# Kernel tuning notes

Measured on AMD Instinct MI355X. Metric: run time of the kernel, lower is better.

## Reference

```python
import jax, jax.numpy as jnp
import numpy as np
from math import sqrt

DIM, RANK = 1024, 32
B, S = 4, 4096

def setup_inputs() -> dict:
    key = jax.random.key(0)
    kx, kq, kk, kv = jax.random.split(key, 4)
    # xavier_uniform bounds
    bq = sqrt(6.0 / (RANK + DIM))
    bv = sqrt(6.0 / (DIM + DIM))
    return {
        "x": jax.random.normal(kx, (B, S, DIM), dtype=jnp.float32),
        "Q": jax.random.uniform(kq, (RANK, DIM), jnp.float32, -bq, bq),
        "K": jax.random.uniform(kk, (RANK, DIM), jnp.float32, -bq, bq),
        "VO": jax.random.uniform(kv, (DIM, DIM), jnp.float32, -bv, bv),
    }

def reference(x, Q, K, VO):
    d = x.shape[-1]
    # low-rank projections: [b,t,r] each (avoid materializing QK^T [d,d] or 4-way einsum blowup)
    xq = jnp.einsum('btd,rd->btr', x, Q)
    xk = jnp.einsum('bud,rd->bur', x, K)
    scores = jnp.einsum('btr,bur->btu', xq, xk) / sqrt(d)
    attn = jax.nn.softmax(scores, axis=2)
    # value aggregation then output projection
    ctx = jnp.einsum('btu,bud->btd', attn, x)
    return jnp.einsum('btd,de->bte', ctx, VO)
```

## Files before the change

### kernel.cpp

```cpp
#include <hip/hip_runtime.h>
#include <hip/hip_bf16.h>

#define DIM  1024
#define RANK 32
#define BATCH 4
#define SEQ  4096
#define MTOT (BATCH * SEQ)

typedef short bf16x8 __attribute__((ext_vector_type(8)));
typedef float f32x4 __attribute__((ext_vector_type(4)));
typedef float f32x16 __attribute__((ext_vector_type(16)));
typedef unsigned short ushort8v __attribute__((ext_vector_type(8)));
typedef unsigned int uint2v __attribute__((ext_vector_type(2)));

__device__ inline unsigned short f2bf(float f) {
    union { float f; unsigned int u; } v; v.f = f;
    return (unsigned short)((v.u + 0x7FFFu + ((v.u >> 16) & 1u)) >> 16);
}

__device__ inline unsigned int pk_bf16(float a, float b) {
    __hip_bfloat162 h = __float22bfloat162_rn(make_float2(a, b));
    unsigned int u; __builtin_memcpy(&u, &h, 4);
    return u;
}

__device__ inline void gl_lds16(const unsigned short* g, unsigned short* l) {
    __builtin_amdgcn_global_load_lds(
        (const __attribute__((address_space(1))) unsigned int*)g,
        (__attribute__((address_space(3))) unsigned int*)l, 16, 0, 0);
}

__global__ __launch_bounds__(256) void k_cvt_qk(const float* __restrict__ Q,
                                                const float* __restrict__ K,
                                                unsigned short* __restrict__ wqk) {
    int i = blockIdx.x * 256 + threadIdx.x;
    int row = i >> 10, col = i & 1023;
    const float SC = 0.045084220027779984f;
    float v = (row < RANK) ? Q[row * DIM + col] * SC : K[(row - RANK) * DIM + col];
    wqk[i] = f2bf(v);
}

__global__ __launch_bounds__(256) void k_transpose_cvt(const float* __restrict__ in,
                                                       unsigned short* __restrict__ out,
                                                       int R, int C) {
    __shared__ float tile[64][65];
    const int tid = threadIdx.x;
    const int c0 = blockIdx.x * 64, r0 = blockIdx.y * 64;
    {
        int c = (tid & 15) * 4;
#pragma unroll
        for (int i = 0; i < 4; ++i) {
            int r = (tid >> 4) + i * 16;
            f32x4 v = *(const f32x4*)(in + (size_t)(r0 + r) * C + c0 + c);
            tile[r][c + 0] = v[0]; tile[r][c + 1] = v[1];
            tile[r][c + 2] = v[2]; tile[r][c + 3] = v[3];
        }
    }
    __syncthreads();
    {
        int r = (tid & 15) * 4;
#pragma unroll
        for (int i = 0; i < 4; ++i) {
            int c = (tid >> 4) + i * 16;
            unsigned short o0 = f2bf(tile[r + 0][c]), o1 = f2bf(tile[r + 1][c]);
            unsigned short o2 = f2bf(tile[r + 2][c]), o3 = f2bf(tile[r + 3][c]);
            unsigned short* p = out + (size_t)(c0 + c) * R + r0 + r;
            p[0] = o0; p[1] = o1; p[2] = o2; p[3] = o3;
        }
    }
}

__global__ __launch_bounds__(256) void k_xbf(const float* __restrict__ x,
                                             unsigned short* __restrict__ xbf) {
    size_t i = ((size_t)blockIdx.x * 256 + threadIdx.x) * 8;
    f32x4 v0 = *(const f32x4*)(x + i);
    f32x4 v1 = *(const f32x4*)(x + i + 4);
    ushort8v o;
    o[0] = f2bf(v0[0]); o[1] = f2bf(v0[1]); o[2] = f2bf(v0[2]); o[3] = f2bf(v0[3]);
    o[4] = f2bf(v1[0]); o[5] = f2bf(v1[1]); o[6] = f2bf(v1[2]); o[7] = f2bf(v1[3]);
    *(ushort8v*)(xbf + i) = o;
}

__global__ __launch_bounds__(256) void k_proj(const unsigned short* __restrict__ xbf,
                                              const unsigned short* __restrict__ wqk,
                                              unsigned short* __restrict__ xqk) {
    __shared__ __align__(16) unsigned short a_lds[128 * 32];
    __shared__ __align__(16) unsigned short w_lds[64 * 32];
    const int tid = threadIdx.x;
    const int w = tid >> 6, lane = tid & 63, l15 = lane & 15, quad = lane >> 4;
    const int wm = w & 1, wn = w >> 1;
    const int rowbase = blockIdx.x * 128;

    f32x4 acc[4][2];
#pragma unroll
    for (int mt = 0; mt < 4; ++mt)
#pragma unroll
        for (int nt = 0; nt < 2; ++nt) acc[mt][nt] = (f32x4){0.f, 0.f, 0.f, 0.f};

    const unsigned short* Ab = xbf + (size_t)(rowbase + w * 32 + (lane >> 2)) * DIM + (lane & 3) * 8;
    const unsigned short* Wb = wqk + (size_t)(w * 16 + (lane >> 2)) * DIM + (lane & 3) * 8;

    for (int k0 = 0; k0 < DIM; k0 += 32) {
        gl_lds16(Ab + k0, &a_lds[(w * 32) * 32]);
        gl_lds16(Ab + (size_t)16 * DIM + k0, &a_lds[(w * 32 + 16) * 32]);
        gl_lds16(Wb + k0, &w_lds[(w * 16) * 32]);
        __syncthreads();
        bf16x8 am[4], bn[2];
#pragma unroll
        for (int mt = 0; mt < 4; ++mt)
            am[mt] = *(const bf16x8*)&a_lds[(wm * 64 + mt * 16 + l15) * 32 + quad * 8];
#pragma unroll
        for (int nt = 0; nt < 2; ++nt)
            bn[nt] = *(const bf16x8*)&w_lds[(wn * 32 + nt * 16 + l15) * 32 + quad * 8];
#pragma unroll
        for (int mt = 0; mt < 4; ++mt)
#pragma unroll
            for (int nt = 0; nt < 2; ++nt)
                acc[mt][nt] = __builtin_amdgcn_mfma_f32_16x16x32_bf16(am[mt], bn[nt], acc[mt][nt], 0, 0, 0);
        __syncthreads();
    }
#pragma unroll
    for (int mt = 0; mt < 4; ++mt)
#pragma unroll
        for (int nt = 0; nt < 2; ++nt)
#pragma unroll
            for (int r = 0; r < 4; ++r) {
                int grow = rowbase + wm * 64 + mt * 16 + quad * 4 + r;
                xqk[(size_t)grow * 64 + wn * 32 + nt * 16 + l15] = f2bf(acc[mt][nt][r]);
            }
}

__global__ __launch_bounds__(256) void k_score(const unsigned short* __restrict__ xqk,
                                               unsigned short* __restrict__ P,
                                               float* __restrict__ den_part) {
    __shared__ __align__(16) unsigned short xk_lds[128 * 32];
    __shared__ __align__(16) unsigned short p_lds[64 * 136];
    __shared__ float denp[4][64];
    const int tid = threadIdx.x;
    const int w = tid >> 6, lane = tid & 63, l31 = lane & 31, half = lane >> 5;
    const int qbase = blockIdx.x * 64;
    const int kc = blockIdx.y;
    const int b = blockIdx.z;

    bf16x8 bq[2][2];
#pragma unroll
    for (int qt = 0; qt < 2; ++qt) {
        const unsigned short* base = xqk + (size_t)(b * SEQ + qbase + qt * 32 + l31) * 64 + half * 8;
        bq[qt][0] = *(const bf16x8*)(base);
        bq[qt][1] = *(const bf16x8*)(base + 16);
    }
    float dacc[2] = {0.f, 0.f};

    const unsigned short* XKb = xqk + (size_t)(b * SEQ + kc * 512 + w * 32 + (lane >> 2)) * 64 + 32 + (lane & 3) * 8;

    for (int it = 0; it < 4; ++it) {
        const int kkey = kc * 512 + it * 128;
        gl_lds16(XKb + (size_t)(it * 128) * 64, &xk_lds[(w * 32) * 32]);
        gl_lds16(XKb + (size_t)(it * 128 + 16) * 64, &xk_lds[(w * 32 + 16) * 32]);
        __syncthreads();

        bf16x8 ak0 = *(const bf16x8*)&xk_lds[(w * 32 + l31) * 32 + half * 8];
        bf16x8 ak1 = *(const bf16x8*)&xk_lds[(w * 32 + l31) * 32 + 16 + half * 8];
        f32x16 z;
#pragma unroll
        for (int i = 0; i < 16; ++i) z[i] = 0.f;
#pragma unroll
        for (int qt = 0; qt < 2; ++qt) {
            f32x16 sc = __builtin_amdgcn_mfma_f32_32x32x16_bf16(ak0, bq[qt][0], z, 0, 0, 0);
            sc = __builtin_amdgcn_mfma_f32_32x32x16_bf16(ak1, bq[qt][1], sc, 0, 0, 0);
#pragma unroll
            for (int g = 0; g < 4; ++g) {
                float e0 = exp2f(sc[4 * g + 0]), e1 = exp2f(sc[4 * g + 1]);
                float e2 = exp2f(sc[4 * g + 2]), e3 = exp2f(sc[4 * g + 3]);
                dacc[qt] += (e0 + e1) + (e2 + e3);
                uint2v dw; dw[0] = pk_bf16(e0, e1); dw[1] = pk_bf16(e2, e3);
                *(uint2v*)&p_lds[(qt * 32 + l31) * 136 + w * 32 + g * 8 + half * 4] = dw;
            }
        }
        __syncthreads();
#pragma unroll
        for (int i = 0; i < 4; ++i) {
            int row = i * 16 + (tid >> 4);
            int col = (tid & 15) * 8;
            ushort8v v = *(const ushort8v*)&p_lds[row * 136 + col];
            *(ushort8v*)(P + (size_t)(b * SEQ + qbase + row) * SEQ + kkey + col) = v;
        }
    }
#pragma unroll
    for (int qt = 0; qt < 2; ++qt) {
        float d = dacc[qt];
        d += __shfl_xor(d, 32);
        if (half == 0) denp[w][qt * 32 + l31] = d;
    }
    __syncthreads();
    if (tid < 64) {
        float s = denp[0][tid] + denp[1][tid] + denp[2][tid] + denp[3][tid];
        den_part[(size_t)kc * MTOT + b * SEQ + qbase + tid] = s;
    }
}

__global__ __launch_bounds__(512, 4) void k_xvo(const unsigned short* __restrict__ vot,
                                                const unsigned short* __restrict__ xbf,
                                                unsigned short* __restrict__ xvoT) {
    __shared__ __align__(16) unsigned short a_lds[128 * 64];
    __shared__ __align__(16) unsigned short b_lds[256 * 64];
    const int tid = threadIdx.x;
    const int w = tid >> 6, lane = tid & 63, l31 = lane & 31, half = lane >> 5;
    const int wm = w & 1, wn = w >> 1;
    const int ubase = blockIdx.x * 256;
    const int ebase = blockIdx.y * 128;
    const int b = blockIdx.z;

    f32x16 acc[2][2];
#pragma unroll
    for (int at = 0; at < 2; ++at)
#pragma unroll
        for (int bt = 0; bt < 2; ++bt)
#pragma unroll
            for (int i = 0; i < 16; ++i) acc[at][bt][i] = 0.f;

    const int sub = lane >> 3;
    const int g = (lane & 7) ^ (sub & 7);
    const int Ra = w * 16 + sub;
    const int Rb = w * 32 + sub;
    const unsigned short* Ap = vot + (size_t)(ebase + Ra) * DIM + g * 8;
    const unsigned short* Bp = xbf + (size_t)(b * SEQ + ubase + Rb) * DIM + g * 8;

    for (int k0 = 0; k0 < DIM; k0 += 64) {
#pragma unroll
        for (int c = 0; c < 2; ++c)
            gl_lds16(Ap + (size_t)(c * 8) * DIM + k0, &a_lds[(w * 16 + c * 8) * 64]);
#pragma unroll
        for (int c = 0; c < 4; ++c)
            gl_lds16(Bp + (size_t)(c * 8) * DIM + k0, &b_lds[(w * 32 + c * 8) * 64]);
        __syncthreads();

        const int abase = (wm * 64 + l31) * 64;
        const int bbase = (wn * 64 + l31) * 64;
#pragma unroll
        for (int ks = 0; ks < 4; ++ks) {
            const int soff = ((ks * 2 + half) ^ (l31 & 7)) * 8;
            bf16x8 a0 = *(const bf16x8*)&a_lds[abase + soff];
            bf16x8 a1 = *(const bf16x8*)&a_lds[abase + 2048 + soff];
            bf16x8 b0 = *(const bf16x8*)&b_lds[bbase + soff];
            bf16x8 b1 = *(const bf16x8*)&b_lds[bbase + 2048 + soff];
            acc[0][0] = __builtin_amdgcn_mfma_f32_32x32x16_bf16(a0, b0, acc[0][0], 0, 0, 0);
            acc[0][1] = __builtin_amdgcn_mfma_f32_32x32x16_bf16(a0, b1, acc[0][1], 0, 0, 0);
            acc[1][0] = __builtin_amdgcn_mfma_f32_32x32x16_bf16(a1, b0, acc[1][0], 0, 0, 0);
            acc[1][1] = __builtin_amdgcn_mfma_f32_32x32x16_bf16(a1, b1, acc[1][1], 0, 0, 0);
        }
        __syncthreads();
    }
#pragma unroll
    for (int at = 0; at < 2; ++at)
#pragma unroll
        for (int bt = 0; bt < 2; ++bt)
#pragma unroll
            for (int reg = 0; reg < 16; ++reg) {
                int lr = wm * 64 + at * 32 + (reg & 3) + 8 * (reg >> 2) + 4 * half;
                int u = ubase + wn * 64 + bt * 32 + l31;
                xvoT[(size_t)(b * DIM + ebase + lr) * SEQ + u] = f2bf(acc[at][bt][reg]);
            }
}

__global__ __launch_bounds__(512, 4) void k_pv(const unsigned short* __restrict__ P,
                                               const unsigned short* __restrict__ xvoT,
                                               const float* __restrict__ den_part,
                                               float* __restrict__ out) {
    __shared__ __align__(16) unsigned short a_lds[128 * 64];
    __shared__ __align__(16) unsigned short b_lds[256 * 64];
    __shared__ float rden[128];
    const int tid = threadIdx.x;
    const int w = tid >> 6, lane = tid & 63, l31 = lane & 31, half = lane >> 5;
    const int wm = w & 1, wn = w >> 1;

    const int p = blockIdx.x;
    const int xcd = p & 7, t = p >> 3;
    const int rowtile = xcd * 16 + (t >> 2);
    const int etile = t & 3;
    const int rowbase = rowtile * 128;
    const int ebase = etile * 256;
    const int b = rowbase >> 12;

    if (tid < 128) {
        float s = 0.f;
#pragma unroll
        for (int i = 0; i < 8; ++i) s += den_part[(size_t)i * MTOT + rowbase + tid];
        rden[tid] = 1.0f / s;
    }

    f32x16 acc[2][2];
#pragma unroll
    for (int at = 0; at < 2; ++at)
#pragma unroll
        for (int bt = 0; bt < 2; ++bt)
#pragma unroll
            for (int i = 0; i < 16; ++i) acc[at][bt][i] = 0.f;

    const int sub = lane >> 3;
    const int g = (lane & 7) ^ (sub & 7);
    const int Ra = w * 16 + sub;
    const int Rb = w * 32 + sub;
    const unsigned short* Ap = P + (size_t)(rowbase + Ra) * SEQ + g * 8;
    const unsigned short* Bp = xvoT + (size_t)(b * DIM + ebase + Rb) * SEQ + g * 8;

    for (int k0 = 0; k0 < SEQ; k0 += 64) {
#pragma unroll
        for (int c = 0; c < 2; ++c)
            gl_lds16(Ap + (size_t)(c * 8) * SEQ + k0, &a_lds[(w * 16 + c * 8) * 64]);
#pragma unroll
        for (int c = 0; c < 4; ++c)
            gl_lds16(Bp + (size_t)(c * 8) * SEQ + k0, &b_lds[(w * 32 + c * 8) * 64]);
        __syncthreads();

        const int abase = (wm * 64 + l31) * 64;
        const int bbase = (wn * 64 + l31) * 64;
#pragma unroll
        for (int ks = 0; ks < 4; ++ks) {
            const int soff = ((ks * 2 + half) ^ (l31 & 7)) * 8;
            bf16x8 a0 = *(const bf16x8*)&a_lds[abase + soff];
            bf16x8 a1 = *(const bf16x8*)&a_lds[abase + 2048 + soff];
            bf16x8 b0 = *(const bf16x8*)&b_lds[bbase + soff];
            bf16x8 b1 = *(const bf16x8*)&b_lds[bbase + 2048 + soff];
            acc[0][0] = __builtin_amdgcn_mfma_f32_32x32x16_bf16(a0, b0, acc[0][0], 0, 0, 0);
            acc[0][1] = __builtin_amdgcn_mfma_f32_32x32x16_bf16(a0, b1, acc[0][1], 0, 0, 0);
            acc[1][0] = __builtin_amdgcn_mfma_f32_32x32x16_bf16(a1, b0, acc[1][0], 0, 0, 0);
            acc[1][1] = __builtin_amdgcn_mfma_f32_32x32x16_bf16(a1, b1, acc[1][1], 0, 0, 0);
        }
        __syncthreads();
    }
#pragma unroll
    for (int at = 0; at < 2; ++at)
#pragma unroll
        for (int bt = 0; bt < 2; ++bt)
#pragma unroll
            for (int reg = 0; reg < 16; ++reg) {
                int lr = wm * 64 + at * 32 + (reg & 3) + 8 * (reg >> 2) + 4 * half;
                int e = ebase + wn * 64 + bt * 32 + l31;
                out[(size_t)(rowbase + lr) * DIM + e] = acc[at][bt][reg] * rden[lr];
            }
}

extern "C" void kernel_launch(void* const* d_in, const int* in_sizes, int n_in,
                              void* d_out, int out_size, void* d_ws, size_t ws_size,
                              hipStream_t stream) {
    const float* x  = (const float*)d_in[0];
    const float* Q  = (const float*)d_in[1];
    const float* K  = (const float*)d_in[2];
    const float* VO = (const float*)d_in[3];
    float* out = (float*)d_out;

    char* ws = (char*)d_ws;
    unsigned short* wqk  = (unsigned short*)(ws + 0);
    unsigned short* vot  = (unsigned short*)(ws + 131072);
    unsigned short* xqk  = (unsigned short*)(ws + 2228224);
    unsigned short* xbf  = (unsigned short*)(ws + 4325376);
    unsigned short* xvoT = (unsigned short*)(ws + 37879808);
    float*          denp = (float*)(ws + 71434240);
    unsigned short* P    = (unsigned short*)(ws + 71958528);

    k_cvt_qk<<<256, 256, 0, stream>>>(Q, K, wqk);
    k_transpose_cvt<<<dim3(16, 16, 1), 256, 0, stream>>>(VO, vot, 1024, 1024);
    k_xbf<<<8192, 256, 0, stream>>>(x, xbf);
    k_proj<<<128, 256, 0, stream>>>(xbf, wqk, xqk);
    k_score<<<dim3(SEQ / 64, 8, BATCH), 256, 0, stream>>>(xqk, P, denp);
    k_xvo<<<dim3(16, 8, BATCH), 512, 0, stream>>>(vot, xbf, xvoT);
    k_pv<<<dim3(512, 1, 1), 512, 0, stream>>>(P, xvoT, denp, out);
}
```

Baseline: 325.3 us.

## Triple-buffer LDS with async prefetch in XVO and PV GEMM kernels

Both bf16 GEMM kernels (x·VO and P·xVO) now keep three LDS stages and prefetch tiles two iterations ahead using direct global-to-LDS loads. Explicit vmcnt waits and raw barriers replace the two __syncthreads per iteration, so global loads overlap MFMA work. MFMA sections are also raised in wave priority. The larger LDS footprint (about 144KB) lowers occupancy, and launch bounds drop from 4 to 2 blocks per SM to match. The hand-counted vmcnt values depend on the exact number of loads each stage issues.

```diff
diff --git a/kernel.cpp b/kernel.cpp
--- a/kernel.cpp
+++ b/kernel.cpp
@@ -199,11 +199,11 @@
     }
 }
 
-__global__ __launch_bounds__(512, 4) void k_xvo(const unsigned short* __restrict__ vot,
+__global__ __launch_bounds__(512, 2) void k_xvo(const unsigned short* __restrict__ vot,
                                                 const unsigned short* __restrict__ xbf,
                                                 unsigned short* __restrict__ xvoT) {
-    __shared__ __align__(16) unsigned short a_lds[128 * 64];
-    __shared__ __align__(16) unsigned short b_lds[256 * 64];
+    __shared__ __align__(16) unsigned short a_lds[3][128 * 64];
+    __shared__ __align__(16) unsigned short b_lds[3][256 * 64];
     const int tid = threadIdx.x;
     const int w = tid >> 6, lane = tid & 63, l31 = lane & 31, half = lane >> 5;
     const int wm = w & 1, wn = w >> 1;
@@ -221,35 +221,57 @@
 
     const int sub = lane >> 3;
     const int g = (lane & 7) ^ (sub & 7);
-    const int Ra = w * 16 + sub;
-    const int Rb = w * 32 + sub;
-    const unsigned short* Ap = vot + (size_t)(ebase + Ra) * DIM + g * 8;
-    const unsigned short* Bp = xbf + (size_t)(b * SEQ + ubase + Rb) * DIM + g * 8;
-
-    for (int k0 = 0; k0 < DIM; k0 += 64) {
+    const unsigned short* Ap = vot + (size_t)(ebase + w * 16 + sub) * DIM + g * 8;
+    const unsigned short* Bp = xbf + (size_t)(b * SEQ + ubase + w * 32 + sub) * DIM + g * 8;
+
+    auto stage = [&](int sb, int k0) {
 #pragma unroll
         for (int c = 0; c < 2; ++c)
-            gl_lds16(Ap + (size_t)(c * 8) * DIM + k0, &a_lds[(w * 16 + c * 8) * 64]);
+            gl_lds16(Ap + (size_t)(c * 8) * DIM + k0, &a_lds[sb][(w * 16 + c * 8) * 64]);
 #pragma unroll
         for (int c = 0; c < 4; ++c)
-            gl_lds16(Bp + (size_t)(c * 8) * DIM + k0, &b_lds[(w * 32 + c * 8) * 64]);
-        __syncthreads();
-
+            gl_lds16(Bp + (size_t)(c * 8) * DIM + k0, &b_lds[sb][(w * 32 + c * 8) * 64]);
+    };
+
+    const int NT = DIM / 64;
+    stage(0, 0);
+    stage(1, 64);
+    int cur = 0;
+    for (int t = 0; t < NT; ++t) {
+        if (t + 2 < NT) {
+            int sb = cur - 1; if (sb < 0) sb = 2;
+            stage(sb, (t + 2) * 64);
+            asm volatile("s_waitcnt vmcnt(12)" ::: "memory");
+        } else if (t + 1 < NT) {
+            asm volatile("s_waitcnt vmcnt(6)" ::: "memory");
+        } else {
+            asm volatile("s_waitcnt vmcnt(0)" ::: "memory");
+        }
+        __builtin_amdgcn_s_barrier();
+        asm volatile("" ::: "memory");
+
+        const unsigned short* al = a_lds[cur];
+        const unsigned short* bl = b_lds[cur];
         const int abase = (wm * 64 + l31) * 64;
         const int bbase = (wn * 64 + l31) * 64;
+        __builtin_amdgcn_s_setprio(1);
 #pragma unroll
         for (int ks = 0; ks < 4; ++ks) {
             const int soff = ((ks * 2 + half) ^ (l31 & 7)) * 8;
-            bf16x8 a0 = *(const bf16x8*)&a_lds[abase + soff];
-            bf16x8 a1 = *(const bf16x8*)&a_lds[abase + 2048 + soff];
-            bf16x8 b0 = *(const bf16x8*)&b_lds[bbase + soff];
-            bf16x8 b1 = *(const bf16x8*)&b_lds[bbase + 2048 + soff];
+            bf16x8 a0 = *(const bf16x8*)&al[abase + soff];
+            bf16x8 a1 = *(const bf16x8*)&al[abase + 2048 + soff];
+            bf16x8 b0 = *(const bf16x8*)&bl[bbase + soff];
+            bf16x8 b1 = *(const bf16x8*)&bl[bbase + 2048 + soff];
             acc[0][0] = __builtin_amdgcn_mfma_f32_32x32x16_bf16(a0, b0, acc[0][0], 0, 0, 0);
             acc[0][1] = __builtin_amdgcn_mfma_f32_32x32x16_bf16(a0, b1, acc[0][1], 0, 0, 0);
             acc[1][0] = __builtin_amdgcn_mfma_f32_32x32x16_bf16(a1, b0, acc[1][0], 0, 0, 0);
             acc[1][1] = __builtin_amdgcn_mfma_f32_32x32x16_bf16(a1, b1, acc[1][1], 0, 0, 0);
         }
-        __syncthreads();
+        __builtin_amdgcn_s_setprio(0);
+        asm volatile("" ::: "memory");
+        __builtin_amdgcn_s_barrier();
+        asm volatile("" ::: "memory");
+        cur = (cur == 2) ? 0 : cur + 1;
     }
 #pragma unroll
     for (int at = 0; at < 2; ++at)
@@ -263,21 +285,21 @@
             }
 }
 
-__global__ __launch_bounds__(512, 4) void k_pv(const unsigned short* __restrict__ P,
+__global__ __launch_bounds__(512, 2) void k_pv(const unsigned short* __restrict__ P,
                                                const unsigned short* __restrict__ xvoT,
                                                const float* __restrict__ den_part,
                                                float* __restrict__ out) {
-    __shared__ __align__(16) unsigned short a_lds[128 * 64];
-    __shared__ __align__(16) unsigned short b_lds[256 * 64];
+    __shared__ __align__(16) unsigned short a_lds[3][128 * 64];
+    __shared__ __align__(16) unsigned short b_lds[3][256 * 64];
     __shared__ float rden[128];
     const int tid = threadIdx.x;
     const int w = tid >> 6, lane = tid & 63, l31 = lane & 31, half = lane >> 5;
     const int wm = w & 1, wn = w >> 1;
 
     const int p = blockIdx.x;
-    const int xcd = p & 7, t = p >> 3;
-    const int rowtile = xcd * 16 + (t >> 2);
-    const int etile = t & 3;
+    const int xcd = p & 7, t0 = p >> 3;
+    const int rowtile = xcd * 16 + (t0 >> 2);
+    const int etile = t0 & 3;
     const int rowbase = rowtile * 128;
     const int ebase = etile * 256;
     const int b = rowbase >> 12;
@@ -288,6 +310,7 @@
         for (int i = 0; i < 8; ++i) s += den_part[(size_t)i * MTOT + rowbase + tid];
         rden[tid] = 1.0f / s;
     }
+    asm volatile("s_waitcnt lgkmcnt(0)" ::: "memory");
 
     f32x16 acc[2][2];
 #pragma unroll
@@ -299,35 +322,57 @@
 
     const int sub = lane >> 3;
     const int g = (lane & 7) ^ (sub & 7);
-    const int Ra = w * 16 + sub;
-    const int Rb = w * 32 + sub;
-    const unsigned short* Ap = P + (size_t)(rowbase + Ra) * SEQ + g * 8;
-    const unsigned short* Bp = xvoT + (size_t)(b * DIM + ebase + Rb) * SEQ + g * 8;
-
-    for (int k0 = 0; k0 < SEQ; k0 += 64) {
+    const unsigned short* Ap = P + (size_t)(rowbase + w * 16 + sub) * SEQ + g * 8;
+    const unsigned short* Bp = xvoT + (size_t)(b * DIM + ebase + w * 32 + sub) * SEQ + g * 8;
+
+    auto stage = [&](int sb, int k0) {
 #pragma unroll
         for (int c = 0; c < 2; ++c)
-            gl_lds16(Ap + (size_t)(c * 8) * SEQ + k0, &a_lds[(w * 16 + c * 8) * 64]);
+            gl_lds16(Ap + (size_t)(c * 8) * SEQ + k0, &a_lds[sb][(w * 16 + c * 8) * 64]);
 #pragma unroll
         for (int c = 0; c < 4; ++c)
-            gl_lds16(Bp + (size_t)(c * 8) * SEQ + k0, &b_lds[(w * 32 + c * 8) * 64]);
-        __syncthreads();
-
+            gl_lds16(Bp + (size_t)(c * 8) * SEQ + k0, &b_lds[sb][(w * 32 + c * 8) * 64]);
+    };
+
+    const int NT = SEQ / 64;
+    stage(0, 0);
+    stage(1, 64);
+    int cur = 0;
+    for (int t = 0; t < NT; ++t) {
+        if (t + 2 < NT) {
+            int sb = cur - 1; if (sb < 0) sb = 2;
+            stage(sb, (t + 2) * 64);
+            asm volatile("s_waitcnt vmcnt(12)" ::: "memory");
+        } else if (t + 1 < NT) {
+            asm volatile("s_waitcnt vmcnt(6)" ::: "memory");
+        } else {
+            asm volatile("s_waitcnt vmcnt(0)" ::: "memory");
+        }
+        __builtin_amdgcn_s_barrier();
+        asm volatile("" ::: "memory");
+
+        const unsigned short* al = a_lds[cur];
+        const unsigned short* bl = b_lds[cur];
         const int abase = (wm * 64 + l31) * 64;
         const int bbase = (wn * 64 + l31) * 64;
+        __builtin_amdgcn_s_setprio(1);
 #pragma unroll
         for (int ks = 0; ks < 4; ++ks) {
             const int soff = ((ks * 2 + half) ^ (l31 & 7)) * 8;
-            bf16x8 a0 = *(const bf16x8*)&a_lds[abase + soff];
-            bf16x8 a1 = *(const bf16x8*)&a_lds[abase + 2048 + soff];
-            bf16x8 b0 = *(const bf16x8*)&b_lds[bbase + soff];
-            bf16x8 b1 = *(const bf16x8*)&b_lds[bbase + 2048 + soff];
+            bf16x8 a0 = *(const bf16x8*)&al[abase + soff];
+            bf16x8 a1 = *(const bf16x8*)&al[abase + 2048 + soff];
+            bf16x8 b0 = *(const bf16x8*)&bl[bbase + soff];
+            bf16x8 b1 = *(const bf16x8*)&bl[bbase + 2048 + soff];
             acc[0][0] = __builtin_amdgcn_mfma_f32_32x32x16_bf16(a0, b0, acc[0][0], 0, 0, 0);
             acc[0][1] = __builtin_amdgcn_mfma_f32_32x32x16_bf16(a0, b1, acc[0][1], 0, 0, 0);
             acc[1][0] = __builtin_amdgcn_mfma_f32_32x32x16_bf16(a1, b0, acc[1][0], 0, 0, 0);
             acc[1][1] = __builtin_amdgcn_mfma_f32_32x32x16_bf16(a1, b1, acc[1][1], 0, 0, 0);
         }
-        __syncthreads();
+        __builtin_amdgcn_s_setprio(0);
+        asm volatile("" ::: "memory");
+        __builtin_amdgcn_s_barrier();
+        asm volatile("" ::: "memory");
+        cur = (cur == 2) ? 0 : cur + 1;
     }
 #pragma unroll
     for (int at = 0; at < 2; ++at)
```

Measured after the change: 391.9 us. 20.5% more time.
